# Kernel tuning notes

Measured on AMD Instinct MI355X. Metric: run time of the kernel, lower is better.

The kernel has to match this reference:

```python
import jax, jax.numpy as jnp
import numpy as np

B, S, TEXT_DIM, VISION_DIM, HIDDEN, HEADS = 4, 2048, 768, 768, 512, 8
HEAD_DIM = HIDDEN // HEADS


def setup_inputs() -> dict:
    key = jax.random.key(0)
    ks = jax.random.split(key, 9)
    s_in = 1.0 / np.sqrt(TEXT_DIM)
    s_h = 1.0 / np.sqrt(HIDDEN)
    return {
        "text_embeds": jax.random.normal(ks[0], (B, S, TEXT_DIM), dtype=jnp.float32),
        "Wq": jax.random.uniform(ks[1], (TEXT_DIM, HIDDEN), jnp.float32, -s_in, s_in),
        "bq": jax.random.uniform(ks[2], (HIDDEN,), jnp.float32, -s_in, s_in),
        "Wk": jax.random.uniform(ks[3], (TEXT_DIM, HIDDEN), jnp.float32, -s_in, s_in),
        "bk": jax.random.uniform(ks[4], (HIDDEN,), jnp.float32, -s_in, s_in),
        "Wv": jax.random.uniform(ks[5], (TEXT_DIM, HIDDEN), jnp.float32, -s_in, s_in),
        "bv": jax.random.uniform(ks[6], (HIDDEN,), jnp.float32, -s_in, s_in),
        "Wo": jax.random.uniform(ks[7], (HIDDEN, VISION_DIM), jnp.float32, -s_h, s_h),
        "bo": jax.random.uniform(ks[8], (VISION_DIM,), jnp.float32, -s_h, s_h),
    }


def reference(text_embeds, Wq, bq, Wk, bk, Wv, bv, Wo, bo):
    b, s, _ = text_embeds.shape
    # QKV projections -> [b, heads, s, head_dim]
    def proj(W, bias):
        y = jnp.einsum("bsd,dh->bsh", text_embeds, W) + bias
        return y.reshape(b, s, HEADS, HEAD_DIM).transpose(0, 2, 1, 3)
    q, k, v = proj(Wq, bq), proj(Wk, bk), proj(Wv, bv)
    scores = jnp.einsum("bhqd,bhkd->bhqk", q, k) / np.sqrt(HEAD_DIM).astype(np.float32)
    weights = jax.nn.softmax(scores, axis=-1)
    attended = jnp.einsum("bhqk,bhkd->bhqd", weights, v)
    attended = attended.transpose(0, 2, 1, 3).reshape(b, s, HIDDEN)
    out = jnp.einsum("bsh,hv->bsv", attended, Wo) + bo
    return jnp.squeeze(out, axis=1) if out.shape[1] == 1 else out
```

## Files before the change

### kernel.cpp

```cpp
#include <hip/hip_runtime.h>
#include <hip/hip_bf16.h>

#define BATCH 4
#define SEQ 2048
#define TDIM 768
#define VDIM 768
#define HID 512
#define NHEADS 8
#define HDIM 64
#define MROWS (BATCH * SEQ)
#define NQKV (3 * HID)

typedef unsigned short ushort_t;
typedef __attribute__((ext_vector_type(8))) short short8;
typedef __attribute__((ext_vector_type(4))) short short4v;
typedef __attribute__((ext_vector_type(4))) float floatx4;

#define QSCALE 0.18033688011112042f

__device__ __forceinline__ ushort_t bf16_rne(float f) {
    unsigned int u = __float_as_uint(f);
    u = (u + 0x7fffu + ((u >> 16) & 1u)) >> 16;
    return (ushort_t)u;
}

__device__ __forceinline__ void async16(const ushort_t* g, ushort_t* l) {
    __builtin_amdgcn_global_load_lds(
        (const __attribute__((address_space(1))) unsigned int*)g,
        (__attribute__((address_space(3))) unsigned int*)l, 16, 0, 0);
}

__global__ __launch_bounds__(256) void conv_x(const float* __restrict__ X,
                                              ushort_t* __restrict__ Xb)
{
    const int i = (blockIdx.x * 256 + threadIdx.x) * 4;
    const floatx4 v = *(const floatx4*)(X + i);
    short4v o;
#pragma unroll
    for (int j = 0; j < 4; ++j) o[j] = (short)bf16_rne(v[j]);
    *(short4v*)(Xb + i) = o;
}

__global__ __launch_bounds__(256) void transp_w(
    const float* __restrict__ Wq, const float* __restrict__ Wk,
    const float* __restrict__ Wv, const float* __restrict__ Wo,
    ushort_t* __restrict__ Wqkvt, ushort_t* __restrict__ Wot)
{
    __shared__ float tile[32][33];
    const int z = blockIdx.z;
    const float* src;
    ushort_t* dst;
    int R, C;
    if (z < 3) {
        src = (z == 0) ? Wq : (z == 1) ? Wk : Wv;
        dst = Wqkvt + (size_t)z * HID * TDIM;
        R = TDIM; C = HID;
    } else {
        src = Wo; dst = Wot; R = HID; C = VDIM;
    }
    const int tx = threadIdx.x & 31, ty = threadIdx.x >> 5;
    const int c0 = blockIdx.x * 32, r0 = blockIdx.y * 32;
    if (c0 >= C || r0 >= R) return;
#pragma unroll
    for (int i = 0; i < 4; ++i)
        tile[ty + i * 8][tx] = src[(size_t)(r0 + ty + i * 8) * C + c0 + tx];
    __syncthreads();
#pragma unroll
    for (int i = 0; i < 4; ++i)
        dst[(size_t)(c0 + ty + i * 8) * R + r0 + tx] = bf16_rne(tile[tx][ty + i * 8]);
}

template<int KD, bool SWAPPED>
__device__ __forceinline__ void gemm128(
    const ushort_t* __restrict__ A, const ushort_t* __restrict__ Bt,
    int m0, int n0, ushort_t* As, ushort_t* Bs, floatx4 (&acc)[4][4])
{
    const int tid  = threadIdx.x;
    const int lane = tid & 63;
    const int w    = tid >> 6;
    const int l15  = lane & 15;
    const int quad = lane >> 4;
    const int wrow = w >> 1;
    const int wcol = w & 1;

    const int srow = lane >> 3;
    const int scol = ((lane & 7) ^ srow) * 8;

    const ushort_t* ga = A  + (size_t)(m0 + w * 32 + srow) * KD + scol;
    const ushort_t* gb = Bt + (size_t)(n0 + w * 32 + srow) * KD + scol;
    ushort_t* la = As + (w * 32) * 64;
    ushort_t* lb = Bs + (w * 32) * 64;

    for (int kt = 0; kt < KD; kt += 64) {
#pragma unroll
        for (int i = 0; i < 4; ++i) {
            async16(ga + (size_t)(i * 8) * KD + kt, la + i * 8 * 64);
            async16(gb + (size_t)(i * 8) * KD + kt, lb + i * 8 * 64);
        }
        __syncthreads();
#pragma unroll
        for (int half = 0; half < 2; ++half) {
            const int kk = ((half * 4 + quad) ^ (l15 & 7)) * 8;
            short8 af[4], bf[4];
#pragma unroll
            for (int t = 0; t < 4; ++t) {
                af[t] = *(const short8*)&As[(wrow * 64 + t * 16 + l15) * 64 + kk];
                bf[t] = *(const short8*)&Bs[(wcol * 64 + t * 16 + l15) * 64 + kk];
            }
#pragma unroll
            for (int mi = 0; mi < 4; ++mi)
#pragma unroll
                for (int ni = 0; ni < 4; ++ni) {
                    if (SWAPPED)
                        acc[mi][ni] = __builtin_amdgcn_mfma_f32_16x16x32_bf16(
                            bf[ni], af[mi], acc[mi][ni], 0, 0, 0);
                    else
                        acc[mi][ni] = __builtin_amdgcn_mfma_f32_16x16x32_bf16(
                            af[mi], bf[ni], acc[mi][ni], 0, 0, 0);
                }
        }
        __syncthreads();
    }
}

__global__ __launch_bounds__(256) void qkv_gemm_mfma(
    const ushort_t* __restrict__ Xb, const ushort_t* __restrict__ Wt,
    const float* __restrict__ bq, const float* __restrict__ bk,
    const float* __restrict__ bv,
    ushort_t* __restrict__ Q, ushort_t* __restrict__ K, ushort_t* __restrict__ V)
{
    __shared__ __align__(16) ushort_t As[128 * 64];
    __shared__ __align__(16) ushort_t Bs[128 * 64];

    const int bx = blockIdx.x;
    const int m0 = blockIdx.y * 128;
    const int n0 = bx * 128;
    const int which = bx >> 2;
    const bool isV = (which == 2);

    floatx4 acc[4][4];
#pragma unroll
    for (int i = 0; i < 4; ++i)
#pragma unroll
        for (int j = 0; j < 4; ++j) acc[i][j] = (floatx4)0.0f;

    if (isV) gemm128<TDIM, false>(Xb, Wt, m0, n0, As, Bs, acc);
    else     gemm128<TDIM, true >(Xb, Wt, m0, n0, As, Bs, acc);

    const int lane = threadIdx.x & 63;
    const int w    = threadIdx.x >> 6;
    const int l15  = lane & 15;
    const int quad = lane >> 4;
    const int wrow = w >> 1;
    const int wcol = w & 1;

    if (!isV) {
        const float* bias = (which == 0) ? bq : bk;
        const float scale = (which == 0) ? QSCALE : 1.0f;
        ushort_t* Out = (which == 0) ? Q : K;
#pragma unroll
        for (int mi = 0; mi < 4; ++mi) {
            const int m = m0 + wrow * 64 + mi * 16 + l15;
            const int b = m >> 11;
            const int s = m & 2047;
#pragma unroll
            for (int ni = 0; ni < 4; ++ni) {
                const int c = (n0 - which * HID) + wcol * 64 + ni * 16 + quad * 4;
                const int h = c >> 6;
                const int d0 = c & 63;
                const floatx4 b4 = *(const floatx4*)(bias + c);
                short4v pk;
#pragma unroll
                for (int r = 0; r < 4; ++r)
                    pk[r] = (short)bf16_rne((acc[mi][ni][r] + b4[r]) * scale);
                *(short4v*)&Out[((size_t)(b * NHEADS + h) * SEQ + s) * HDIM + d0] = pk;
            }
        }
    } else {
#pragma unroll
        for (int ni = 0; ni < 4; ++ni) {
            const int c = (n0 - 2 * HID) + wcol * 64 + ni * 16 + l15;
            const int h = c >> 6;
            const int d = c & 63;
            const float b1 = bv[c];
#pragma unroll
            for (int mi = 0; mi < 4; ++mi) {
                const int mb = m0 + wrow * 64 + mi * 16 + quad * 4;
                const int b = mb >> 11;
                const int s0 = mb & 2047;
                short4v pk;
#pragma unroll
                for (int r = 0; r < 4; ++r)
                    pk[r] = (short)bf16_rne(acc[mi][ni][r] + b1);
                *(short4v*)&V[((size_t)(b * NHEADS + h) * HDIM + d) * SEQ + s0] = pk;
            }
        }
    }
}

__global__ __launch_bounds__(512) void flash_attn_mfma(
    const ushort_t* __restrict__ Q, const ushort_t* __restrict__ K,
    const ushort_t* __restrict__ Vt, ushort_t* __restrict__ Att)
{
    __shared__ __align__(16) ushort_t Ks[2][64 * 64];
    __shared__ __align__(16) ushort_t Vs[2][64 * 64];

    const int tid  = threadIdx.x;
    const int lane = tid & 63;
    const int w    = tid >> 6;
    const int l15  = lane & 15;
    const int quad = lane >> 4;

    const int bh = blockIdx.y;
    const int b  = bh >> 3;
    const int h  = bh & 7;
    const int q0 = blockIdx.x * 128;

    const ushort_t* Qb = Q  + (size_t)bh * SEQ * HDIM;
    const ushort_t* Kb = K  + (size_t)bh * SEQ * HDIM;
    const ushort_t* Vb = Vt + (size_t)bh * HDIM * SEQ;

    short8 qf0, qf1;
    {
        const ushort_t* qrow = Qb + (size_t)(q0 + w * 16 + l15) * HDIM + quad * 8;
        qf0 = *(const short8*)(qrow);
        qf1 = *(const short8*)(qrow + 32);
    }

    floatx4 of[4];
#pragma unroll
    for (int t = 0; t < 4; ++t) of[t] = (floatx4)0.0f;
    floatx4 ofl = (floatx4)0.0f;

    short8 ones;
#pragma unroll
    for (int j = 0; j < 8; ++j) ones[j] = (short)0x3F80;

    const floatx4 z4 = (floatx4)0.0f;

    const int srow = lane >> 3;
    const int scol = ((lane & 7) ^ srow) * 8;
    const ushort_t* gk = Kb + (size_t)(w * 8 + srow) * HDIM + scol;
    const ushort_t* gv = Vb + (size_t)(w * 8 + srow) * SEQ + scol;
    ushort_t* lk0 = &Ks[0][w * 8 * 64];
    ushort_t* lk1 = &Ks[1][w * 8 * 64];
    ushort_t* lv0 = &Vs[0][w * 8 * 64];
    ushort_t* lv1 = &Vs[1][w * 8 * 64];

    const int off0 = (quad ^ (l15 & 7)) * 8;
    const int off1 = off0 ^ 32;

    auto tile = [&](const ushort_t* Kt, const ushort_t* Vt_) {
        floatx4 sacc[4];
        __builtin_amdgcn_s_setprio(1);
#pragma unroll
        for (int t = 0; t < 4; ++t) {
            const short8 kf0 = *(const short8*)&Kt[(t * 16 + l15) * 64 + off0];
            const short8 kf1 = *(const short8*)&Kt[(t * 16 + l15) * 64 + off1];
            floatx4 a = z4;
            a = __builtin_amdgcn_mfma_f32_16x16x32_bf16(kf0, qf0, a, 0, 0, 0);
            a = __builtin_amdgcn_mfma_f32_16x16x32_bf16(kf1, qf1, a, 0, 0, 0);
            sacc[t] = a;
        }
        __builtin_amdgcn_s_setprio(0);

        unsigned w0[4], w1[4];
#pragma unroll
        for (int t = 0; t < 4; ++t) {
            const float p0 = __builtin_amdgcn_exp2f(sacc[t][0]);
            const float p1 = __builtin_amdgcn_exp2f(sacc[t][1]);
            const float p2 = __builtin_amdgcn_exp2f(sacc[t][2]);
            const float p3 = __builtin_amdgcn_exp2f(sacc[t][3]);
            asm("v_cvt_pk_bf16_f32 %0, %1, %2" : "=v"(w0[t]) : "v"(p0), "v"(p1));
            asm("v_cvt_pk_bf16_f32 %0, %1, %2" : "=v"(w1[t]) : "v"(p2), "v"(p3));
        }

        unsigned a0 = w0[0], b0 = w0[1];
        asm("v_permlane32_swap_b32 %0, %1" : "+v"(a0), "+v"(b0));
        asm("v_permlane16_swap_b32 %0, %1" : "+v"(a0), "+v"(b0));
        unsigned a1 = w1[0], b1 = w1[1];
        asm("v_permlane32_swap_b32 %0, %1" : "+v"(a1), "+v"(b1));
        asm("v_permlane16_swap_b32 %0, %1" : "+v"(a1), "+v"(b1));
        unsigned a2 = w0[2], b2 = w0[3];
        asm("v_permlane32_swap_b32 %0, %1" : "+v"(a2), "+v"(b2));
        asm("v_permlane16_swap_b32 %0, %1" : "+v"(a2), "+v"(b2));
        unsigned a3 = w1[2], b3 = w1[3];
        asm("v_permlane32_swap_b32 %0, %1" : "+v"(a3), "+v"(b3));
        asm("v_permlane16_swap_b32 %0, %1" : "+v"(a3), "+v"(b3));

        union { unsigned u[4]; short8 s; } P0, P1;
        P0.u[0] = a0; P0.u[1] = a1; P0.u[2] = b0; P0.u[3] = b1;
        P1.u[0] = a2; P1.u[1] = a3; P1.u[2] = b2; P1.u[3] = b3;
        const short8 pf0 = P0.s;
        const short8 pf1 = P1.s;

        __builtin_amdgcn_s_setprio(1);
        ofl = __builtin_amdgcn_mfma_f32_16x16x32_bf16(ones, pf0, ofl, 0, 0, 0);
        ofl = __builtin_amdgcn_mfma_f32_16x16x32_bf16(ones, pf1, ofl, 0, 0, 0);
#pragma unroll
        for (int t = 0; t < 4; ++t) {
            const short8 vf0 = *(const short8*)&Vt_[(t * 16 + l15) * 64 + off0];
            const short8 vf1 = *(const short8*)&Vt_[(t * 16 + l15) * 64 + off1];
            of[t] = __builtin_amdgcn_mfma_f32_16x16x32_bf16(vf0, pf0, of[t], 0, 0, 0);
            of[t] = __builtin_amdgcn_mfma_f32_16x16x32_bf16(vf1, pf1, of[t], 0, 0, 0);
        }
        __builtin_amdgcn_s_setprio(0);
    };

    async16(gk, lk0);
    async16(gv, lv0);

    for (int kt = 0; kt < SEQ; kt += 128) {
        __syncthreads();
        async16(gk + (size_t)(kt + 64) * HDIM, lk1);
        async16(gv + (kt + 64), lv1);
        tile(Ks[0], Vs[0]);

        __syncthreads();
        if (kt + 128 < SEQ) {
            async16(gk + (size_t)(kt + 128) * HDIM, lk0);
            async16(gv + (kt + 128), lv0);
        }
        tile(Ks[1], Vs[1]);
    }

    const float inv = 1.f / ofl[0];

    const int s = q0 + w * 16 + l15;
    ushort_t* arow = Att + ((size_t)(b * SEQ + s)) * HID + h * HDIM;
#pragma unroll
    for (int t = 0; t < 4; ++t) {
        short4v pk;
#pragma unroll
        for (int r = 0; r < 4; ++r) pk[r] = (short)bf16_rne(of[t][r] * inv);
        *(short4v*)&arow[t * 16 + quad * 4] = pk;
    }
}

__global__ __launch_bounds__(256) void out_gemm_mfma(
    const ushort_t* __restrict__ Attb, const ushort_t* __restrict__ Wot,
    const float* __restrict__ bo, float* __restrict__ Y)
{
    __shared__ __align__(16) ushort_t As[128 * 64];
    __shared__ __align__(16) ushort_t Bs[128 * 64];

    const int m0 = blockIdx.y * 128;
    const int n0 = blockIdx.x * 128;

    floatx4 acc[4][4];
#pragma unroll
    for (int i = 0; i < 4; ++i)
#pragma unroll
        for (int j = 0; j < 4; ++j) acc[i][j] = (floatx4)0.0f;

    gemm128<HID, true>(Attb, Wot, m0, n0, As, Bs, acc);

    const int lane = threadIdx.x & 63;
    const int w    = threadIdx.x >> 6;
    const int l15  = lane & 15;
    const int quad = lane >> 4;
    const int wrow = w >> 1;
    const int wcol = w & 1;

#pragma unroll
    for (int mi = 0; mi < 4; ++mi) {
        const int m = m0 + wrow * 64 + mi * 16 + l15;
#pragma unroll
        for (int ni = 0; ni < 4; ++ni) {
            const int nb = n0 + wcol * 64 + ni * 16 + quad * 4;
            const floatx4 b4 = *(const floatx4*)(bo + nb);
            floatx4 o;
#pragma unroll
            for (int r = 0; r < 4; ++r) o[r] = acc[mi][ni][r] + b4[r];
            *(floatx4*)&Y[(size_t)m * VDIM + nb] = o;
        }
    }
}

extern "C" void kernel_launch(void* const* d_in, const int* in_sizes, int n_in,
                              void* d_out, int out_size, void* d_ws, size_t ws_size,
                              hipStream_t stream)
{
    const float* text = (const float*)d_in[0];
    const float* Wq = (const float*)d_in[1];
    const float* bq = (const float*)d_in[2];
    const float* Wk = (const float*)d_in[3];
    const float* bk = (const float*)d_in[4];
    const float* Wv = (const float*)d_in[5];
    const float* bv = (const float*)d_in[6];
    const float* Wo = (const float*)d_in[7];
    const float* bo = (const float*)d_in[8];
    float* out = (float*)d_out;

    ushort_t* Xb    = (ushort_t*)d_ws;
    ushort_t* Wqkvt = Xb + (size_t)MROWS * TDIM;
    ushort_t* Wot   = Wqkvt + (size_t)NQKV * TDIM;
    ushort_t* Qw    = Wot + (size_t)VDIM * HID;
    ushort_t* Kw    = Qw + (size_t)MROWS * HID;
    ushort_t* Vtw   = Kw + (size_t)MROWS * HID;
    ushort_t* Attb  = Vtw + (size_t)MROWS * HID;

    conv_x<<<dim3(MROWS * TDIM / 1024), 256, 0, stream>>>(text, Xb);
    transp_w<<<dim3(24, 24, 4), 256, 0, stream>>>(Wq, Wk, Wv, Wo, Wqkvt, Wot);
    qkv_gemm_mfma<<<dim3(12, 64), 256, 0, stream>>>(Xb, Wqkvt, bq, bk, bv, Qw, Kw, Vtw);
    flash_attn_mfma<<<dim3(16, 32), 512, 0, stream>>>(Qw, Kw, Vtw, Attb);
    out_gemm_mfma<<<dim3(6, 64), 256, 0, stream>>>(Attb, Wot, bo, out);
}
```

Measured before the change: 185.5 us.

## Switch flash attention to 32x32x16 MFMA with 256-query blocks

Rewrites the attention inner loop to use 32x32x16 bf16 MFMA instructions, with each wave processing 32 query rows, so each block now covers 256 queries. The softmax denominator is accumulated with scalar adds and a cross-half shuffle instead of an extra MFMA against a ones vector. This increases K/V reuse per LDS read and removes MFMA work, but halves the grid to 256 blocks and raises register pressure, which may reduce latency hiding.

New measurement: 192.6 us. 1.04x slower.

```diff
diff --git a/kernel.cpp b/kernel.cpp
--- a/kernel.cpp
+++ b/kernel.cpp
@@ -15,6 +15,7 @@
 typedef __attribute__((ext_vector_type(8))) short short8;
 typedef __attribute__((ext_vector_type(4))) short short4v;
 typedef __attribute__((ext_vector_type(4))) float floatx4;
+typedef __attribute__((ext_vector_type(16))) float floatx16;
 
 #define QSCALE 0.18033688011112042f
 
@@ -208,35 +209,31 @@
     const int tid  = threadIdx.x;
     const int lane = tid & 63;
     const int w    = tid >> 6;
-    const int l15  = lane & 15;
-    const int quad = lane >> 4;
+    const int l31  = lane & 31;
+    const int hi   = lane >> 5;
+    const int r7   = l31 & 7;
 
     const int bh = blockIdx.y;
     const int b  = bh >> 3;
     const int h  = bh & 7;
-    const int q0 = blockIdx.x * 128;
+    const int q0 = blockIdx.x * 256;
 
     const ushort_t* Qb = Q  + (size_t)bh * SEQ * HDIM;
     const ushort_t* Kb = K  + (size_t)bh * SEQ * HDIM;
     const ushort_t* Vb = Vt + (size_t)bh * HDIM * SEQ;
 
-    short8 qf0, qf1;
+    short8 qf[4];
     {
-        const ushort_t* qrow = Qb + (size_t)(q0 + w * 16 + l15) * HDIM + quad * 8;
-        qf0 = *(const short8*)(qrow);
-        qf1 = *(const short8*)(qrow + 32);
-    }
-
-    floatx4 of[4];
-#pragma unroll
-    for (int t = 0; t < 4; ++t) of[t] = (floatx4)0.0f;
-    floatx4 ofl = (floatx4)0.0f;
-
-    short8 ones;
-#pragma unroll
-    for (int j = 0; j < 8; ++j) ones[j] = (short)0x3F80;
-
-    const floatx4 z4 = (floatx4)0.0f;
+        const ushort_t* qrow = Qb + (size_t)(q0 + w * 32 + l31) * HDIM + hi * 8;
+#pragma unroll
+        for (int d = 0; d < 4; ++d) qf[d] = *(const short8*)(qrow + d * 16);
+    }
+
+    floatx16 of0 = (floatx16)0.0f;
+    floatx16 of1 = (floatx16)0.0f;
+    float l_run = 0.f;
+
+    const floatx16 z16 = (floatx16)0.0f;
 
     const int srow = lane >> 3;
     const int scol = ((lane & 7) ^ srow) * 8;
@@ -247,62 +244,73 @@
     ushort_t* lv0 = &Vs[0][w * 8 * 64];
     ushort_t* lv1 = &Vs[1][w * 8 * 64];
 
-    const int off0 = (quad ^ (l15 & 7)) * 8;
-    const int off1 = off0 ^ 32;
-
     auto tile = [&](const ushort_t* Kt, const ushort_t* Vt_) {
-        floatx4 sacc[4];
+        floatx16 sacc0 = z16, sacc1 = z16;
         __builtin_amdgcn_s_setprio(1);
 #pragma unroll
-        for (int t = 0; t < 4; ++t) {
-            const short8 kf0 = *(const short8*)&Kt[(t * 16 + l15) * 64 + off0];
-            const short8 kf1 = *(const short8*)&Kt[(t * 16 + l15) * 64 + off1];
-            floatx4 a = z4;
-            a = __builtin_amdgcn_mfma_f32_16x16x32_bf16(kf0, qf0, a, 0, 0, 0);
-            a = __builtin_amdgcn_mfma_f32_16x16x32_bf16(kf1, qf1, a, 0, 0, 0);
-            sacc[t] = a;
+        for (int d = 0; d < 4; ++d) {
+            const int sl = ((2 * d + hi) ^ r7) * 8;
+            const short8 kf0 = *(const short8*)&Kt[l31 * 64 + sl];
+            const short8 kf1 = *(const short8*)&Kt[(32 + l31) * 64 + sl];
+            sacc0 = __builtin_amdgcn_mfma_f32_32x32x16_bf16(kf0, qf[d], sacc0, 0, 0, 0);
+            sacc1 = __builtin_amdgcn_mfma_f32_32x32x16_bf16(kf1, qf[d], sacc1, 0, 0, 0);
         }
         __builtin_amdgcn_s_setprio(0);
 
-        unsigned w0[4], w1[4];
-#pragma unroll
-        for (int t = 0; t < 4; ++t) {
-            const float p0 = __builtin_amdgcn_exp2f(sacc[t][0]);
-            const float p1 = __builtin_amdgcn_exp2f(sacc[t][1]);
-            const float p2 = __builtin_amdgcn_exp2f(sacc[t][2]);
-            const float p3 = __builtin_amdgcn_exp2f(sacc[t][3]);
-            asm("v_cvt_pk_bf16_f32 %0, %1, %2" : "=v"(w0[t]) : "v"(p0), "v"(p1));
-            asm("v_cvt_pk_bf16_f32 %0, %1, %2" : "=v"(w1[t]) : "v"(p2), "v"(p3));
-        }
-
-        unsigned a0 = w0[0], b0 = w0[1];
-        asm("v_permlane32_swap_b32 %0, %1" : "+v"(a0), "+v"(b0));
-        asm("v_permlane16_swap_b32 %0, %1" : "+v"(a0), "+v"(b0));
-        unsigned a1 = w1[0], b1 = w1[1];
-        asm("v_permlane32_swap_b32 %0, %1" : "+v"(a1), "+v"(b1));
-        asm("v_permlane16_swap_b32 %0, %1" : "+v"(a1), "+v"(b1));
-        unsigned a2 = w0[2], b2 = w0[3];
-        asm("v_permlane32_swap_b32 %0, %1" : "+v"(a2), "+v"(b2));
-        asm("v_permlane16_swap_b32 %0, %1" : "+v"(a2), "+v"(b2));
-        unsigned a3 = w1[2], b3 = w1[3];
-        asm("v_permlane32_swap_b32 %0, %1" : "+v"(a3), "+v"(b3));
-        asm("v_permlane16_swap_b32 %0, %1" : "+v"(a3), "+v"(b3));
-
-        union { unsigned u[4]; short8 s; } P0, P1;
-        P0.u[0] = a0; P0.u[1] = a1; P0.u[2] = b0; P0.u[3] = b1;
-        P1.u[0] = a2; P1.u[1] = a3; P1.u[2] = b2; P1.u[3] = b3;
-        const short8 pf0 = P0.s;
-        const short8 pf1 = P1.s;
+        unsigned ua[8], ub[8];
+        float rs = 0.f;
+#pragma unroll
+        for (int g = 0; g < 4; ++g) {
+            const float p0 = __builtin_amdgcn_exp2f(sacc0[g * 4 + 0]);
+            const float p1 = __builtin_amdgcn_exp2f(sacc0[g * 4 + 1]);
+            const float p2 = __builtin_amdgcn_exp2f(sacc0[g * 4 + 2]);
+            const float p3 = __builtin_amdgcn_exp2f(sacc0[g * 4 + 3]);
+            rs += (p0 + p1) + (p2 + p3);
+            asm("v_cvt_pk_bf16_f32 %0, %1, %2" : "=v"(ua[2 * g])     : "v"(p0), "v"(p1));
+            asm("v_cvt_pk_bf16_f32 %0, %1, %2" : "=v"(ua[2 * g + 1]) : "v"(p2), "v"(p3));
+        }
+#pragma unroll
+        for (int g = 0; g < 4; ++g) {
+            const float p0 = __builtin_amdgcn_exp2f(sacc1[g * 4 + 0]);
+            const float p1 = __builtin_amdgcn_exp2f(sacc1[g * 4 + 1]);
+            const float p2 = __builtin_amdgcn_exp2f(sacc1[g * 4 + 2]);
+            const float p3 = __builtin_amdgcn_exp2f(sacc1[g * 4 + 3]);
+            rs += (p0 + p1) + (p2 + p3);
+            asm("v_cvt_pk_bf16_f32 %0, %1, %2" : "=v"(ub[2 * g])     : "v"(p0), "v"(p1));
+            asm("v_cvt_pk_bf16_f32 %0, %1, %2" : "=v"(ub[2 * g + 1]) : "v"(p2), "v"(p3));
+        }
+        l_run += rs;
+
+        short8 pfr[4];
+#pragma unroll
+        for (int t = 0; t < 2; ++t) {
+            unsigned x0 = ua[4 * t + 0], y0 = ua[4 * t + 2];
+            asm("v_permlane32_swap_b32 %0, %1" : "+v"(x0), "+v"(y0));
+            unsigned x1 = ua[4 * t + 1], y1 = ua[4 * t + 3];
+            asm("v_permlane32_swap_b32 %0, %1" : "+v"(x1), "+v"(y1));
+            union { unsigned u[4]; short8 s8; } P;
+            P.u[0] = x0; P.u[1] = x1; P.u[2] = y0; P.u[3] = y1;
+            pfr[t] = P.s8;
+        }
+#pragma unroll
+        for (int t = 0; t < 2; ++t) {
+            unsigned x0 = ub[4 * t + 0], y0 = ub[4 * t + 2];
+            asm("v_permlane32_swap_b32 %0, %1" : "+v"(x0), "+v"(y0));
+            unsigned x1 = ub[4 * t + 1], y1 = ub[4 * t + 3];
+            asm("v_permlane32_swap_b32 %0, %1" : "+v"(x1), "+v"(y1));
+            union { unsigned u[4]; short8 s8; } P;
+            P.u[0] = x0; P.u[1] = x1; P.u[2] = y0; P.u[3] = y1;
+            pfr[2 + t] = P.s8;
+        }
 
         __builtin_amdgcn_s_setprio(1);
-        ofl = __builtin_amdgcn_mfma_f32_16x16x32_bf16(ones, pf0, ofl, 0, 0, 0);
-        ofl = __builtin_amdgcn_mfma_f32_16x16x32_bf16(ones, pf1, ofl, 0, 0, 0);
-#pragma unroll
-        for (int t = 0; t < 4; ++t) {
-            const short8 vf0 = *(const short8*)&Vt_[(t * 16 + l15) * 64 + off0];
-            const short8 vf1 = *(const short8*)&Vt_[(t * 16 + l15) * 64 + off1];
-            of[t] = __builtin_amdgcn_mfma_f32_16x16x32_bf16(vf0, pf0, of[t], 0, 0, 0);
-            of[t] = __builtin_amdgcn_mfma_f32_16x16x32_bf16(vf1, pf1, of[t], 0, 0, 0);
+#pragma unroll
+        for (int ks = 0; ks < 4; ++ks) {
+            const int sl = ((2 * ks + hi) ^ r7) * 8;
+            const short8 vf0 = *(const short8*)&Vt_[l31 * 64 + sl];
+            const short8 vf1 = *(const short8*)&Vt_[(32 + l31) * 64 + sl];
+            of0 = __builtin_amdgcn_mfma_f32_32x32x16_bf16(vf0, pfr[ks], of0, 0, 0, 0);
+            of1 = __builtin_amdgcn_mfma_f32_32x32x16_bf16(vf1, pfr[ks], of1, 0, 0, 0);
         }
         __builtin_amdgcn_s_setprio(0);
     };
@@ -324,16 +332,21 @@
         tile(Ks[1], Vs[1]);
     }
 
-    const float inv = 1.f / ofl[0];
-
-    const int s = q0 + w * 16 + l15;
+    l_run += __shfl_xor(l_run, 32);
+    const float inv = 1.f / l_run;
+
+    const int s = q0 + w * 32 + l31;
     ushort_t* arow = Att + ((size_t)(b * SEQ + s)) * HID + h * HDIM;
 #pragma unroll
-    for (int t = 0; t < 4; ++t) {
-        short4v pk;
-#pragma unroll
-        for (int r = 0; r < 4; ++r) pk[r] = (short)bf16_rne(of[t][r] * inv);
-        *(short4v*)&arow[t * 16 + quad * 4] = pk;
+    for (int rq = 0; rq < 4; ++rq) {
+        short4v pk0, pk1;
+#pragma unroll
+        for (int j = 0; j < 4; ++j) {
+            pk0[j] = (short)bf16_rne(of0[rq * 4 + j] * inv);
+            pk1[j] = (short)bf16_rne(of1[rq * 4 + j] * inv);
+        }
+        *(short4v*)&arow[rq * 8 + hi * 4]      = pk0;
+        *(short4v*)&arow[32 + rq * 8 + hi * 4] = pk1;
     }
 }
 
@@ -403,6 +416,6 @@
     conv_x<<<dim3(MROWS * TDIM / 1024), 256, 0, stream>>>(text, Xb);
     transp_w<<<dim3(24, 24, 4), 256, 0, stream>>>(Wq, Wk, Wv, Wo, Wqkvt, Wot);
     qkv_gemm_mfma<<<dim3(12, 64), 256, 0, stream>>>(Xb, Wqkvt, bq, bk, bv, Qw, Kw, Vtw);
-    flash_attn_mfma<<<dim3(16, 32), 512, 0, stream>>>(Qw, Kw, Vtw, Attb);
+    flash_attn_mfma<<<dim3(8, 32), 512, 0, stream>>>(Qw, Kw, Vtw, Attb);
     out_gemm_mfma<<<dim3(6, 64), 256, 0, stream>>>(Attb, Wot, bo, out);
 }
```
